# Optimization experiments

Measured on AMD Instinct MI355X. Metric: run time of the kernel, lower is better.

The kernel has to match this reference:

```python
import jax, jax.numpy as jnp
import numpy as np

N_NODES = 50000
N_EDGES = 1_600_000
IN_DIM = 512
HIDDEN = 512
OUT_DIM = 128
K = 10
ALPHA = 0.1


def setup_inputs() -> dict:
    key = jax.random.key(0)
    ks = jax.random.split(key, 7)
    x = jax.random.normal(ks[0], (N_NODES, IN_DIM), dtype=jnp.float32)
    edge_index = jax.random.randint(ks[1], (2, N_EDGES), 0, N_NODES, dtype=jnp.int64)
    s_in = 1.0 / np.sqrt(IN_DIM)
    s_h = 1.0 / np.sqrt(HIDDEN)
    lin_in_w = jax.random.uniform(ks[2], (HIDDEN, IN_DIM), jnp.float32, -s_in, s_in)
    lin_in_b = jax.random.uniform(ks[3], (HIDDEN,), jnp.float32, -s_in, s_in)
    lin_out_w = jax.random.uniform(ks[4], (OUT_DIM, HIDDEN), jnp.float32, -s_h, s_h)
    lin_out_b = jax.random.uniform(ks[5], (OUT_DIM,), jnp.float32, -s_h, s_h)
    # GPR init: alpha*(1-alpha)^k, normalized
    w = np.array([ALPHA * (1 - ALPHA) ** k for k in range(K + 1)], dtype=np.float32)
    gpr_weights = jnp.asarray(w / w.sum())
    return {
        "x": x, "edge_index": edge_index,
        "lin_in_w": lin_in_w, "lin_in_b": lin_in_b,
        "lin_out_w": lin_out_w, "lin_out_b": lin_out_b,
        "gpr_weights": gpr_weights,
    }


def reference(x, edge_index, lin_in_w, lin_in_b, lin_out_w, lin_out_b, gpr_weights):
    n = x.shape[0]
    loops = jnp.arange(n, dtype=edge_index.dtype)
    row = jnp.concatenate([edge_index[0], loops])  # [E+n]
    col = jnp.concatenate([edge_index[1], loops])
    # degree over rows (edge_index_sl[0]), clamped to >=1
    deg = jax.ops.segment_sum(jnp.ones_like(row, dtype=x.dtype), row, num_segments=n)
    dis = jnp.clip(deg, 1.0) ** -0.5  # deg^-0.5, [n]

    h = jax.nn.relu(x @ lin_in_w.T + lin_in_b)  # [n, hidden] (dropout = identity in eval)
    w = jax.nn.softmax(gpr_weights)  # [K+1]

    def step(carry, wk):
        h_prop, acc = carry
        hs = h_prop * dis[:, None]
        h_prop = jax.ops.segment_sum(hs[col], row, num_segments=n) * dis[:, None]
        return (h_prop, acc + wk * h_prop), None

    (_, h_final), _ = jax.lax.scan(step, (h, w[0] * h), w[1:])
    return h_final @ lin_out_w.T + lin_out_b
```

## Files before the change

kernel.cpp:

```cpp
#include <hip/hip_runtime.h>


#define SLOTS 96
#define NB2   98
#define BCAP  18432
#define CHUNK 4096

typedef __attribute__((ext_vector_type(8))) short short8;
typedef __attribute__((ext_vector_type(4))) float f32x4;

__device__ inline ushort f2bf(float f) {
    uint x = __float_as_uint(f);
    return (ushort)((x + 0x7fffu + ((x >> 16) & 1u)) >> 16);
}
__device__ inline float bflo(uint u) { return __uint_as_float(u << 16); }
__device__ inline float bfhi(uint u) { return __uint_as_float(u & 0xffff0000u); }

__device__ __forceinline__ void glds16(const ushort* g, ushort* l) {
    __builtin_amdgcn_global_load_lds(
        (const __attribute__((address_space(1))) void*)g,
        (__attribute__((address_space(3))) void*)l, 16, 0, 0);
}

__global__ void init_kernel(int* __restrict__ gcur, int ngc,
                            ushort* __restrict__ yAll, size_t ystride, int zrow,
                            const float* __restrict__ gpr, float* __restrict__ w11) {
    const int gid = blockIdx.x * blockDim.x + threadIdx.x;
    const int stride = gridDim.x * blockDim.x;
    if (gid == 0) {
        float m = gpr[0];
        for (int i = 1; i < 11; ++i) m = fmaxf(m, gpr[i]);
        float e[11], s = 0.f;
        for (int i = 0; i < 11; ++i) { e[i] = expf(gpr[i] - m); s += e[i]; }
        float inv = 1.f / s;
        for (int i = 0; i < 11; ++i) w11[i] = e[i] * inv;
    }
    for (int i = gid; i < ngc; i += stride) gcur[i] = 0;
    for (int i = gid; i < 11 * 128; i += stride) {
        int k = i >> 7, d = i & 127;
        yAll[(size_t)k * ystride + (size_t)zrow * 128 + d] = 0;
    }
}

__global__ __launch_bounds__(512) void partition_kernel(
    const int* __restrict__ row, const int* __restrict__ col,
    int* __restrict__ gcur, uint* __restrict__ bbuf, int E) {
    __shared__ int cnt[128];
    __shared__ int base[128];
    __shared__ int gbase[128];
    __shared__ uint sbuf[CHUNK];
    const int tid = threadIdx.x;
    const int e0 = blockIdx.x * CHUNK;
    if (tid < 128) cnt[tid] = 0;
    __syncthreads();
    int myb[8]; int myp[8]; uint mye[8];
#pragma unroll
    for (int j = 0; j < 8; ++j) {
        int i = e0 + tid + j * 512;
        myb[j] = -1;
        if (i < E) {
            int r = row[i];
            int c = col[i];
            myb[j] = r >> 9;
            mye[j] = ((uint)(r & 511) << 16) | (uint)c;
            myp[j] = atomicAdd(&cnt[myb[j]], 1);
        }
    }
    __syncthreads();
    if (tid < 128) base[tid] = cnt[tid];
    __syncthreads();
    for (int off = 1; off < 128; off <<= 1) {
        int v = 0;
        if (tid < 128 && tid >= off) v = base[tid - off];
        __syncthreads();
        if (tid < 128) base[tid] += v;
        __syncthreads();
    }
    if (tid < 128) base[tid] -= cnt[tid];
    __syncthreads();
    if (tid < NB2 && cnt[tid] > 0) gbase[tid] = atomicAdd(&gcur[tid], cnt[tid]);
    __syncthreads();
#pragma unroll
    for (int j = 0; j < 8; ++j)
        if (myb[j] >= 0) sbuf[base[myb[j]] + myp[j]] = mye[j];
    __syncthreads();
    const int wv = tid >> 6, lane = tid & 63;
    for (int b = wv; b < NB2; b += 8) {
        const int len = cnt[b], src = base[b], dst = gbase[b];
        for (int i = lane; i < len; i += 64) {
            int d = dst + i;
            if (d < BCAP) bbuf[(size_t)b * BCAP + d] = sbuf[src + i];
        }
    }
}

__global__ __launch_bounds__(1024) void expand2_kernel(
    const int* __restrict__ gcur, const uint* __restrict__ bbuf,
    ushort* __restrict__ col_s, int* __restrict__ deg,
    float* __restrict__ dis, float* __restrict__ dis2, float* __restrict__ rdis,
    int n) {
    __shared__ int cur[128];
    const int b = blockIdx.x >> 2;
    const int q = blockIdx.x & 3;
    const int tid = threadIdx.x;
    if (tid < 128) cur[tid] = 0;
    __syncthreads();
    int cb = gcur[b];
    if (cb > BCAP) cb = BCAP;
    const size_t bb = (size_t)b * BCAP;
    const int rlo = q * 128, rhi = rlo + 128;
    for (int i = tid; i < cb; i += 1024) {
        uint e = bbuf[bb + i];
        int rl = (int)(e >> 16);
        if (rl >= rlo && rl < rhi) {
            int p = atomicAdd(&cur[rl - rlo], 1);
            if (p < SLOTS)
                col_s[((size_t)(b * 512 + rl)) * SLOTS + p] = (ushort)(e & 0xffffu);
        }
    }
    __syncthreads();
    if (tid < 128) {
        int r = b * 512 + rlo + tid;
        if (r < n) {
            int d = cur[tid];
            deg[r] = d;
            float fd = (float)(d + 1);
            float di = rsqrtf(fd);
            dis[r] = di;
            dis2[r] = di * di;
            rdis[r] = sqrtf(fd);
            int pstart = d < SLOTS ? d : SLOTS;
            int pend = (pstart + 7) & ~7;
            if (pend > SLOTS) pend = SLOTS;
            ushort* cp = col_s + (size_t)r * SLOTS;
            for (int p = pstart; p < pend; ++p) cp[p] = (ushort)n;
        }
    }
}

__global__ void cvt_all_kernel(const float* __restrict__ x,
                               const float* __restrict__ win,
                               const float* __restrict__ wout,
                               ushort* __restrict__ x_bf,
                               ushort* __restrict__ win_bf,
                               ushort* __restrict__ wout_bf,
                               int nx_src8, int nx8, int nw18, int nw28) {
    const int gid = blockIdx.x * blockDim.x + threadIdx.x;
    const int stride = gridDim.x * blockDim.x;
    const int tot = nx8 + nw18 + nw28;
    for (int i = gid; i < tot; i += stride) {
        const float* src;
        ushort* dst;
        int idx;
        if (i < nx8) {
            if (i >= nx_src8) {
                short8 z = (short8)0;
                *reinterpret_cast<short8*>(x_bf + (size_t)i * 8) = z;
                continue;
            }
            src = x; dst = x_bf; idx = i;
        } else if (i < nx8 + nw18) {
            src = win; dst = win_bf; idx = i - nx8;
        } else {
            src = wout; dst = wout_bf; idx = i - nx8 - nw18;
        }
        const float4* s = reinterpret_cast<const float4*>(src + (size_t)idx * 8);
        float4 a = s[0], b = s[1];
        short8 o;
        o[0] = (short)f2bf(a.x); o[1] = (short)f2bf(a.y);
        o[2] = (short)f2bf(a.z); o[3] = (short)f2bf(a.w);
        o[4] = (short)f2bf(b.x); o[5] = (short)f2bf(b.y);
        o[6] = (short)f2bf(b.z); o[7] = (short)f2bf(b.w);
        *reinterpret_cast<short8*>(dst + (size_t)idx * 8) = o;
    }
}

__global__ __launch_bounds__(512) void gemm1_kernel(
    const ushort* __restrict__ A, const ushort* __restrict__ B,
    const float* __restrict__ bias, ushort* __restrict__ outH, int M) {
    __shared__ __align__(16) ushort As[128 * 32];
    __shared__ __align__(16) ushort Bs[256 * 32];
    const int tid = threadIdx.x;
    const int lane = tid & 63;
    const int w = tid >> 6;
    const int wm = (w >> 2) * 64, wn = (w & 3) * 64;
    const int bm = blockIdx.y * 128, bn = blockIdx.x * 256;
    const int lrow = lane & 15, lk8 = (lane >> 4) * 8;

    f32x4 acc[4][4];
#pragma unroll
    for (int i = 0; i < 4; ++i)
#pragma unroll
        for (int j = 0; j < 4; ++j) acc[i][j] = (f32x4)(0.f);

    const int arow = 16 * w + (lane >> 2);
    const int acol = (lane & 3) * 8;
    const ushort* gA = A + (size_t)(bm + arow) * 512 + acol;
    const ushort* gB0 = B + (size_t)(bn + 32 * w + (lane >> 2)) * 512 + acol;
    const ushort* gB1 = gB0 + (size_t)16 * 512;
    ushort* lA = As + w * 512;
    ushort* lB0 = Bs + w * 1024;
    ushort* lB1 = Bs + w * 1024 + 512;

    for (int k0 = 0; k0 < 512; k0 += 32) {
        glds16(gA + k0, lA);
        glds16(gB0 + k0, lB0);
        glds16(gB1 + k0, lB1);
        __syncthreads();
        short8 af[4], bfr[4];
#pragma unroll
        for (int mf = 0; mf < 4; ++mf)
            af[mf] = *reinterpret_cast<const short8*>(As + (wm + mf * 16 + lrow) * 32 + lk8);
#pragma unroll
        for (int nf = 0; nf < 4; ++nf)
            bfr[nf] = *reinterpret_cast<const short8*>(Bs + (wn + nf * 16 + lrow) * 32 + lk8);
#pragma unroll
        for (int mf = 0; mf < 4; ++mf)
#pragma unroll
            for (int nf = 0; nf < 4; ++nf)
                acc[mf][nf] = __builtin_amdgcn_mfma_f32_16x16x32_bf16(af[mf], bfr[nf], acc[mf][nf], 0, 0, 0);
        __syncthreads();
    }

#pragma unroll
    for (int mf = 0; mf < 4; ++mf) {
#pragma unroll
        for (int nf = 0; nf < 4; ++nf) {
            const int col = bn + wn + nf * 16 + lrow;
#pragma unroll
            for (int r = 0; r < 4; ++r) {
                const int row = bm + wm + mf * 16 + (lane >> 4) * 4 + r;
                if (row < M) {
                    float v = fmaxf(acc[mf][nf][r] + bias[col], 0.f);
                    outH[(size_t)row * 512 + col] = f2bf(v);
                }
            }
        }
    }
}

__global__ __launch_bounds__(256) void gemm2_kernel(
    const ushort* __restrict__ A, const ushort* __restrict__ B,
    const float* __restrict__ dis, ushort* __restrict__ outY, int M) {
    __shared__ __align__(16) ushort As[128 * 32];
    __shared__ __align__(16) ushort Bs[128 * 32];
    const int tid = threadIdx.x;
    const int lane = tid & 63;
    const int w = tid >> 6;
    const int wm = (w >> 1) * 64, wn = (w & 1) * 64;
    const int bm = blockIdx.x * 128;
    const int lrow = lane & 15, lk8 = (lane >> 4) * 8;

    f32x4 acc[4][4];
#pragma unroll
    for (int i = 0; i < 4; ++i)
#pragma unroll
        for (int j = 0; j < 4; ++j) acc[i][j] = (f32x4)(0.f);

    const int sub = 32 * w + (lane >> 2);
    const int acol = (lane & 3) * 8;
    const ushort* gA0 = A + (size_t)(bm + sub) * 512 + acol;
    const ushort* gA1 = gA0 + (size_t)16 * 512;
    const ushort* gB0 = B + (size_t)sub * 512 + acol;
    const ushort* gB1 = gB0 + (size_t)16 * 512;
    ushort* lA0 = As + w * 1024;
    ushort* lA1 = As + w * 1024 + 512;
    ushort* lB0 = Bs + w * 1024;
    ushort* lB1 = Bs + w * 1024 + 512;

    for (int k0 = 0; k0 < 512; k0 += 32) {
        glds16(gA0 + k0, lA0);
        glds16(gA1 + k0, lA1);
        glds16(gB0 + k0, lB0);
        glds16(gB1 + k0, lB1);
        __syncthreads();
        short8 af[4], bfr[4];
#pragma unroll
        for (int mf = 0; mf < 4; ++mf)
            af[mf] = *reinterpret_cast<const short8*>(As + (wm + mf * 16 + lrow) * 32 + lk8);
#pragma unroll
        for (int nf = 0; nf < 4; ++nf)
            bfr[nf] = *reinterpret_cast<const short8*>(Bs + (wn + nf * 16 + lrow) * 32 + lk8);
#pragma unroll
        for (int mf = 0; mf < 4; ++mf)
#pragma unroll
            for (int nf = 0; nf < 4; ++nf)
                acc[mf][nf] = __builtin_amdgcn_mfma_f32_16x16x32_bf16(af[mf], bfr[nf], acc[mf][nf], 0, 0, 0);
        __syncthreads();
    }

#pragma unroll
    for (int mf = 0; mf < 4; ++mf) {
#pragma unroll
        for (int nf = 0; nf < 4; ++nf) {
            const int col = wn + nf * 16 + lrow;
#pragma unroll
            for (int r = 0; r < 4; ++r) {
                const int row = bm + wm + mf * 16 + (lane >> 4) * 4 + r;
                if (row < M)
                    outY[(size_t)row * 128 + col] = f2bf(dis[row] * acc[mf][nf][r]);
            }
        }
    }
}

__global__ __launch_bounds__(256) void spmm128_kernel(
    const int* __restrict__ deg, const ushort* __restrict__ col_s,
    const float* __restrict__ dis2,
    const ushort* __restrict__ y_old, ushort* __restrict__ y_new, int n) {
    int wid = (blockIdx.x * 256 + threadIdx.x) >> 6;
    if (wid >= n) return;
    wid = __builtin_amdgcn_readfirstlane(wid);
    const int lane = threadIdx.x & 63;
    int cnt = deg[wid];
    if (cnt > SLOTS) cnt = SLOTS;
    const int cnt8 = (cnt + 7) & ~7;
    const ushort* __restrict__ cp = col_s + (size_t)wid * SLOTS;
    const uint* __restrict__ Y = reinterpret_cast<const uint*>(y_old);
    float s0a = 0.f, s1a = 0.f, s0b = 0.f, s1b = 0.f;
    int t = 0;
    for (; t + 16 <= cnt8; t += 16) {
        int c[16];
        uint v[16];
#pragma unroll
        for (int j = 0; j < 16; ++j) c[j] = (int)cp[t + j];
#pragma unroll
        for (int j = 0; j < 16; ++j) v[j] = Y[(size_t)c[j] * 64 + lane];
#pragma unroll
        for (int j = 0; j < 16; ++j) {
            if (j & 1) { s0b += bflo(v[j]); s1b += bfhi(v[j]); }
            else       { s0a += bflo(v[j]); s1a += bfhi(v[j]); }
        }
    }
    if (t < cnt8) {
        int c[8];
        uint v[8];
#pragma unroll
        for (int j = 0; j < 8; ++j) c[j] = (int)cp[t + j];
#pragma unroll
        for (int j = 0; j < 8; ++j) v[j] = Y[(size_t)c[j] * 64 + lane];
#pragma unroll
        for (int j = 0; j < 8; ++j) {
            if (j & 1) { s0b += bflo(v[j]); s1b += bfhi(v[j]); }
            else       { s0a += bflo(v[j]); s1a += bfhi(v[j]); }
        }
    }
    const uint u = Y[(size_t)wid * 64 + lane];
    const float d2 = dis2[wid];
    const float y0 = d2 * (bflo(u) + (s0a + s0b));
    const float y1 = d2 * (bfhi(u) + (s1a + s1b));
    reinterpret_cast<uint*>(y_new)[(size_t)wid * 64 + lane] =
        (uint)f2bf(y0) | ((uint)f2bf(y1) << 16);
}

__global__ __launch_bounds__(256) void spmm_last_kernel(
    const int* __restrict__ deg, const ushort* __restrict__ col_s,
    const float* __restrict__ dis2, const float* __restrict__ rdis,
    const ushort* __restrict__ yAll, size_t ystride_dw,
    const float* __restrict__ w11, const float* __restrict__ bout,
    float* __restrict__ outp, int n) {
    int wid = (blockIdx.x * 256 + threadIdx.x) >> 6;
    if (wid >= n) return;
    wid = __builtin_amdgcn_readfirstlane(wid);
    const int lane = threadIdx.x & 63;
    const uint* __restrict__ Y9 = reinterpret_cast<const uint*>(yAll) + 9 * ystride_dw;
    int cnt = deg[wid];
    if (cnt > SLOTS) cnt = SLOTS;
    const int cnt8 = (cnt + 7) & ~7;
    const ushort* __restrict__ cp = col_s + (size_t)wid * SLOTS;
    float s0a = 0.f, s1a = 0.f, s0b = 0.f, s1b = 0.f;
    int t = 0;
    for (; t + 16 <= cnt8; t += 16) {
        int c[16];
        uint v[16];
#pragma unroll
        for (int j = 0; j < 16; ++j) c[j] = (int)cp[t + j];
#pragma unroll
        for (int j = 0; j < 16; ++j) v[j] = Y9[(size_t)c[j] * 64 + lane];
#pragma unroll
        for (int j = 0; j < 16; ++j) {
            if (j & 1) { s0b += bflo(v[j]); s1b += bfhi(v[j]); }
            else       { s0a += bflo(v[j]); s1a += bfhi(v[j]); }
        }
    }
    if (t < cnt8) {
        int c[8];
        uint v[8];
#pragma unroll
        for (int j = 0; j < 8; ++j) c[j] = (int)cp[t + j];
#pragma unroll
        for (int j = 0; j < 8; ++j) v[j] = Y9[(size_t)c[j] * 64 + lane];
#pragma unroll
        for (int j = 0; j < 8; ++j) {
            if (j & 1) { s0b += bflo(v[j]); s1b += bfhi(v[j]); }
            else       { s0a += bflo(v[j]); s1a += bfhi(v[j]); }
        }
    }
    const uint u9 = Y9[(size_t)wid * 64 + lane];
    const float d2 = dis2[wid];
    const float y10_0 = d2 * (bflo(u9) + (s0a + s0b));
    const float y10_1 = d2 * (bfhi(u9) + (s1a + s1b));
    const float w10 = w11[10];
    float s0 = w10 * y10_0, s1 = w10 * y10_1;
    const uint* __restrict__ Y = reinterpret_cast<const uint*>(yAll);
#pragma unroll
    for (int k = 0; k < 10; ++k) {
        const uint v = Y[k * ystride_dw + (size_t)wid * 64 + lane];
        const float wk = w11[k];
        s0 = fmaf(wk, bflo(v), s0);
        s1 = fmaf(wk, bfhi(v), s1);
    }
    const float r = rdis[wid];
    float2 o;
    o.x = fmaf(s0, r, bout[lane * 2 + 0]);
    o.y = fmaf(s1, r, bout[lane * 2 + 1]);
    *reinterpret_cast<float2*>(outp + (size_t)wid * 128 + lane * 2) = o;
}

extern "C" void kernel_launch(void* const* d_in, const int* in_sizes, int n_in,
                              void* d_out, int out_size, void* d_ws, size_t ws_size,
                              hipStream_t stream) {
    const float* x    = (const float*)d_in[0];
    const int*   ei   = (const int*)d_in[1];
    const float* win  = (const float*)d_in[2];
    const float* bin  = (const float*)d_in[3];
    const float* wout = (const float*)d_in[4];
    const float* bout = (const float*)d_in[5];
    const float* gpr  = (const float*)d_in[6];
    float* out = (float*)d_out;

    const int n = in_sizes[0] / 512;
    const int E = in_sizes[1] / 2;
    const int Mpad = ((n + 127) / 128) * 128;
    const int NPAD = NB2 * 512;

    char* ws = (char*)d_ws;
    size_t off = 0;
    auto take = [&](size_t bytes) -> char* {
        char* p = ws + off;
        off += (bytes + 511) & ~(size_t)511;
        return p;
    };
    int*    deg     = (int*)take((size_t)n * sizeof(int));
    float*  dis     = (float*)take((size_t)n * sizeof(float));
    float*  dis2    = (float*)take((size_t)n * sizeof(float));
    float*  rdis    = (float*)take((size_t)n * sizeof(float));
    float*  w11     = (float*)take(16 * sizeof(float));
    int*    gcur    = (int*)take(128 * sizeof(int));
    uint*   bbuf    = (uint*)take((size_t)NB2 * BCAP * sizeof(uint));
    ushort* col_s   = (ushort*)take((size_t)NPAD * SLOTS * sizeof(ushort));
    ushort* x_bf    = (ushort*)take((size_t)Mpad * 512 * sizeof(ushort));
    ushort* win_bf  = (ushort*)take((size_t)512 * 512 * sizeof(ushort));
    ushort* wout_bf = (ushort*)take((size_t)128 * 512 * sizeof(ushort));
    ushort* h_bf    = (ushort*)take((size_t)Mpad * 512 * sizeof(ushort));
    const size_t ystride = (size_t)Mpad * 128;
    ushort* yAll    = (ushort*)take(11 * ystride * sizeof(ushort));

    const int* rowp = ei;
    const int* colp = ei + E;

    init_kernel<<<64, 256, 0, stream>>>(gcur, 128, yAll, ystride, n, gpr, w11);
    partition_kernel<<<(E + CHUNK - 1) / CHUNK, 512, 0, stream>>>(rowp, colp, gcur, bbuf, E);
    expand2_kernel<<<NB2 * 4, 1024, 0, stream>>>(gcur, bbuf, col_s, deg, dis, dis2, rdis, n);

    cvt_all_kernel<<<2048, 256, 0, stream>>>(x, win, wout, x_bf, win_bf, wout_bf,
                                             n * 64, Mpad * 64, 512 * 64, 128 * 64);

    dim3 g1(2, Mpad / 128);
    gemm1_kernel<<<g1, 512, 0, stream>>>(x_bf, win_bf, bin, h_bf, n);

    gemm2_kernel<<<Mpad / 128, 256, 0, stream>>>(h_bf, wout_bf, dis, yAll, n);

    const int spmm_blocks = (n + 3) / 4;
    for (int k = 1; k <= 9; ++k) {
        spmm128_kernel<<<spmm_blocks, 256, 0, stream>>>(
            deg, col_s, dis2, yAll + (size_t)(k - 1) * ystride, yAll + (size_t)k * ystride, n);
    }

    spmm_last_kernel<<<spmm_blocks, 256, 0, stream>>>(
        deg, col_s, dis2, rdis, yAll, ystride / 2, w11, bout, out, n);
}
```

Before: 631.6 us.

## Split propagation features into four 32-column slices for cache-resident SpMM

Stores the propagated feature matrix as four separate 32-column slices, each 64 bytes per row, and runs the full 10-step propagation chain per slice. Each wave splits into four 16-lane groups that gather different neighbours, then combines the partial sums with cross-lane shuffles. The aim is to keep each slice's working set (about 3.2 MB) resident in L2/LLC so random neighbour gathers hit cache instead of HBM. The cost is four times as many kernel launches, four re-reads of the column index lists, and only 16 of 64 lanes doing the final stores.

```diff
diff --git a/kernel.cpp b/kernel.cpp
--- a/kernel.cpp
+++ b/kernel.cpp
@@ -23,7 +23,7 @@
 }
 
 __global__ void init_kernel(int* __restrict__ gcur, int ngc,
-                            ushort* __restrict__ yAll, size_t ystride, int zrow,
+                            uint* __restrict__ yAll, size_t ss32, int zrow,
                             const float* __restrict__ gpr, float* __restrict__ w11) {
     const int gid = blockIdx.x * blockDim.x + threadIdx.x;
     const int stride = gridDim.x * blockDim.x;
@@ -36,9 +36,9 @@
         for (int i = 0; i < 11; ++i) w11[i] = e[i] * inv;
     }
     for (int i = gid; i < ngc; i += stride) gcur[i] = 0;
-    for (int i = gid; i < 11 * 128; i += stride) {
-        int k = i >> 7, d = i & 127;
-        yAll[(size_t)k * ystride + (size_t)zrow * 128 + d] = 0;
+    for (int i = gid; i < 44 * 16; i += stride) {
+        int sk = i >> 4, f = i & 15;
+        yAll[(size_t)sk * ss32 + (size_t)zrow * 16 + f] = 0;
     }
 }
 
@@ -241,7 +241,8 @@
 
 __global__ __launch_bounds__(256) void gemm2_kernel(
     const ushort* __restrict__ A, const ushort* __restrict__ B,
-    const float* __restrict__ dis, ushort* __restrict__ outY, int M) {
+    const float* __restrict__ dis, ushort* __restrict__ outY,
+    size_t chain16, int M) {
     __shared__ __align__(16) ushort As[128 * 32];
     __shared__ __align__(16) ushort Bs[128 * 32];
     const int tid = threadIdx.x;
@@ -294,127 +295,126 @@
 #pragma unroll
         for (int nf = 0; nf < 4; ++nf) {
             const int col = wn + nf * 16 + lrow;
+            const size_t sbase = (size_t)(col >> 5) * chain16 + (col & 31);
 #pragma unroll
             for (int r = 0; r < 4; ++r) {
                 const int row = bm + wm + mf * 16 + (lane >> 4) * 4 + r;
                 if (row < M)
-                    outY[(size_t)row * 128 + col] = f2bf(dis[row] * acc[mf][nf][r]);
+                    outY[sbase + (size_t)row * 32] = f2bf(dis[row] * acc[mf][nf][r]);
             }
         }
     }
 }
 
-__global__ __launch_bounds__(256) void spmm128_kernel(
+__global__ __launch_bounds__(256) void spmm_slice_kernel(
     const int* __restrict__ deg, const ushort* __restrict__ col_s,
     const float* __restrict__ dis2,
-    const ushort* __restrict__ y_old, ushort* __restrict__ y_new, int n) {
+    const uint* __restrict__ y_old, uint* __restrict__ y_new, int n) {
     int wid = (blockIdx.x * 256 + threadIdx.x) >> 6;
     if (wid >= n) return;
     wid = __builtin_amdgcn_readfirstlane(wid);
     const int lane = threadIdx.x & 63;
+    const int grp = lane >> 4, fl = lane & 15;
     int cnt = deg[wid];
     if (cnt > SLOTS) cnt = SLOTS;
     const int cnt8 = (cnt + 7) & ~7;
     const ushort* __restrict__ cp = col_s + (size_t)wid * SLOTS;
-    const uint* __restrict__ Y = reinterpret_cast<const uint*>(y_old);
-    float s0a = 0.f, s1a = 0.f, s0b = 0.f, s1b = 0.f;
+    float s0 = 0.f, s1 = 0.f;
     int t = 0;
     for (; t + 16 <= cnt8; t += 16) {
-        int c[16];
-        uint v[16];
-#pragma unroll
-        for (int j = 0; j < 16; ++j) c[j] = (int)cp[t + j];
-#pragma unroll
-        for (int j = 0; j < 16; ++j) v[j] = Y[(size_t)c[j] * 64 + lane];
-#pragma unroll
-        for (int j = 0; j < 16; ++j) {
-            if (j & 1) { s0b += bflo(v[j]); s1b += bfhi(v[j]); }
-            else       { s0a += bflo(v[j]); s1a += bfhi(v[j]); }
-        }
+        const int myc = (int)cp[t + (lane & 15)];
+        int c[4];
+        uint v[4];
+#pragma unroll
+        for (int i = 0; i < 4; ++i) c[i] = __shfl(myc, i * 4 + grp);
+#pragma unroll
+        for (int i = 0; i < 4; ++i) v[i] = y_old[(size_t)c[i] * 16 + fl];
+#pragma unroll
+        for (int i = 0; i < 4; ++i) { s0 += bflo(v[i]); s1 += bfhi(v[i]); }
     }
     if (t < cnt8) {
-        int c[8];
-        uint v[8];
-#pragma unroll
-        for (int j = 0; j < 8; ++j) c[j] = (int)cp[t + j];
-#pragma unroll
-        for (int j = 0; j < 8; ++j) v[j] = Y[(size_t)c[j] * 64 + lane];
-#pragma unroll
-        for (int j = 0; j < 8; ++j) {
-            if (j & 1) { s0b += bflo(v[j]); s1b += bfhi(v[j]); }
-            else       { s0a += bflo(v[j]); s1a += bfhi(v[j]); }
-        }
-    }
-    const uint u = Y[(size_t)wid * 64 + lane];
+        const int myc = (int)cp[t + (lane & 7)];
+        int c[2];
+        uint v[2];
+#pragma unroll
+        for (int i = 0; i < 2; ++i) c[i] = __shfl(myc, i * 4 + grp);
+#pragma unroll
+        for (int i = 0; i < 2; ++i) v[i] = y_old[(size_t)c[i] * 16 + fl];
+#pragma unroll
+        for (int i = 0; i < 2; ++i) { s0 += bflo(v[i]); s1 += bfhi(v[i]); }
+    }
+    s0 += __shfl_xor(s0, 16); s1 += __shfl_xor(s1, 16);
+    s0 += __shfl_xor(s0, 32); s1 += __shfl_xor(s1, 32);
+    const uint u = y_old[(size_t)wid * 16 + fl];
     const float d2 = dis2[wid];
-    const float y0 = d2 * (bflo(u) + (s0a + s0b));
-    const float y1 = d2 * (bfhi(u) + (s1a + s1b));
-    reinterpret_cast<uint*>(y_new)[(size_t)wid * 64 + lane] =
-        (uint)f2bf(y0) | ((uint)f2bf(y1) << 16);
-}
-
-__global__ __launch_bounds__(256) void spmm_last_kernel(
+    const float y0 = d2 * (bflo(u) + s0);
+    const float y1 = d2 * (bfhi(u) + s1);
+    if (lane < 16)
+        y_new[(size_t)wid * 16 + fl] = (uint)f2bf(y0) | ((uint)f2bf(y1) << 16);
+}
+
+__global__ __launch_bounds__(256) void spmm_last_slice_kernel(
     const int* __restrict__ deg, const ushort* __restrict__ col_s,
     const float* __restrict__ dis2, const float* __restrict__ rdis,
-    const ushort* __restrict__ yAll, size_t ystride_dw,
+    const uint* __restrict__ yChain, size_t ss32,
     const float* __restrict__ w11, const float* __restrict__ bout,
-    float* __restrict__ outp, int n) {
+    float* __restrict__ outp, int colbase, int n) {
     int wid = (blockIdx.x * 256 + threadIdx.x) >> 6;
     if (wid >= n) return;
     wid = __builtin_amdgcn_readfirstlane(wid);
     const int lane = threadIdx.x & 63;
-    const uint* __restrict__ Y9 = reinterpret_cast<const uint*>(yAll) + 9 * ystride_dw;
+    const int grp = lane >> 4, fl = lane & 15;
+    const uint* __restrict__ Y9 = yChain + 9 * ss32;
     int cnt = deg[wid];
     if (cnt > SLOTS) cnt = SLOTS;
     const int cnt8 = (cnt + 7) & ~7;
     const ushort* __restrict__ cp = col_s + (size_t)wid * SLOTS;
-    float s0a = 0.f, s1a = 0.f, s0b = 0.f, s1b = 0.f;
+    float s0 = 0.f, s1 = 0.f;
     int t = 0;
     for (; t + 16 <= cnt8; t += 16) {
-        int c[16];
-        uint v[16];
-#pragma unroll
-        for (int j = 0; j < 16; ++j) c[j] = (int)cp[t + j];
-#pragma unroll
-        for (int j = 0; j < 16; ++j) v[j] = Y9[(size_t)c[j] * 64 + lane];
-#pragma unroll
-        for (int j = 0; j < 16; ++j) {
-            if (j & 1) { s0b += bflo(v[j]); s1b += bfhi(v[j]); }
-            else       { s0a += bflo(v[j]); s1a += bfhi(v[j]); }
-        }
+        const int myc = (int)cp[t + (lane & 15)];
+        int c[4];
+        uint v[4];
+#pragma unroll
+        for (int i = 0; i < 4; ++i) c[i] = __shfl(myc, i * 4 + grp);
+#pragma unroll
+        for (int i = 0; i < 4; ++i) v[i] = Y9[(size_t)c[i] * 16 + fl];
+#pragma unroll
+        for (int i = 0; i < 4; ++i) { s0 += bflo(v[i]); s1 += bfhi(v[i]); }
     }
     if (t < cnt8) {
-        int c[8];
-        uint v[8];
-#pragma unroll
-        for (int j = 0; j < 8; ++j) c[j] = (int)cp[t + j];
-#pragma unroll
-        for (int j = 0; j < 8; ++j) v[j] = Y9[(size_t)c[j] * 64 + lane];
-#pragma unroll
-        for (int j = 0; j < 8; ++j) {
-            if (j & 1) { s0b += bflo(v[j]); s1b += bfhi(v[j]); }
-            else       { s0a += bflo(v[j]); s1a += bfhi(v[j]); }
-        }
-    }
-    const uint u9 = Y9[(size_t)wid * 64 + lane];
+        const int myc = (int)cp[t + (lane & 7)];
+        int c[2];
+        uint v[2];
+#pragma unroll
+        for (int i = 0; i < 2; ++i) c[i] = __shfl(myc, i * 4 + grp);
+#pragma unroll
+        for (int i = 0; i < 2; ++i) v[i] = Y9[(size_t)c[i] * 16 + fl];
+#pragma unroll
+        for (int i = 0; i < 2; ++i) { s0 += bflo(v[i]); s1 += bfhi(v[i]); }
+    }
+    s0 += __shfl_xor(s0, 16); s1 += __shfl_xor(s1, 16);
+    s0 += __shfl_xor(s0, 32); s1 += __shfl_xor(s1, 32);
+    const uint u9 = Y9[(size_t)wid * 16 + fl];
     const float d2 = dis2[wid];
-    const float y10_0 = d2 * (bflo(u9) + (s0a + s0b));
-    const float y10_1 = d2 * (bfhi(u9) + (s1a + s1b));
+    const float y10_0 = d2 * (bflo(u9) + s0);
+    const float y10_1 = d2 * (bfhi(u9) + s1);
     const float w10 = w11[10];
-    float s0 = w10 * y10_0, s1 = w10 * y10_1;
-    const uint* __restrict__ Y = reinterpret_cast<const uint*>(yAll);
+    float a0 = w10 * y10_0, a1 = w10 * y10_1;
 #pragma unroll
     for (int k = 0; k < 10; ++k) {
-        const uint v = Y[k * ystride_dw + (size_t)wid * 64 + lane];
+        const uint v = yChain[k * ss32 + (size_t)wid * 16 + fl];
         const float wk = w11[k];
-        s0 = fmaf(wk, bflo(v), s0);
-        s1 = fmaf(wk, bfhi(v), s1);
+        a0 = fmaf(wk, bflo(v), a0);
+        a1 = fmaf(wk, bfhi(v), a1);
     }
     const float r = rdis[wid];
+    const int cc = colbase + fl * 2;
     float2 o;
-    o.x = fmaf(s0, r, bout[lane * 2 + 0]);
-    o.y = fmaf(s1, r, bout[lane * 2 + 1]);
-    *reinterpret_cast<float2*>(outp + (size_t)wid * 128 + lane * 2) = o;
+    o.x = fmaf(a0, r, bout[cc + 0]);
+    o.y = fmaf(a1, r, bout[cc + 1]);
+    if (lane < 16)
+        *reinterpret_cast<float2*>(outp + (size_t)wid * 128 + cc) = o;
 }
 
 extern "C" void kernel_launch(void* const* d_in, const int* in_sizes, int n_in,
@@ -433,6 +433,9 @@
     const int E = in_sizes[1] / 2;
     const int Mpad = ((n + 127) / 128) * 128;
     const int NPAD = NB2 * 512;
+    const size_t ss32 = (size_t)Mpad * 16;
+    const size_t chain32 = 11 * ss32;
+    const size_t chain16 = 2 * chain32;
 
     char* ws = (char*)d_ws;
     size_t off = 0;
@@ -453,13 +456,12 @@
     ushort* win_bf  = (ushort*)take((size_t)512 * 512 * sizeof(ushort));
     ushort* wout_bf = (ushort*)take((size_t)128 * 512 * sizeof(ushort));
     ushort* h_bf    = (ushort*)take((size_t)Mpad * 512 * sizeof(ushort));
-    const size_t ystride = (size_t)Mpad * 128;
-    ushort* yAll    = (ushort*)take(11 * ystride * sizeof(ushort));
+    uint*   yAll    = (uint*)take(4 * chain32 * sizeof(uint));
 
     const int* rowp = ei;
     const int* colp = ei + E;
 
-    init_kernel<<<64, 256, 0, stream>>>(gcur, 128, yAll, ystride, n, gpr, w11);
+    init_kernel<<<64, 256, 0, stream>>>(gcur, 128, yAll, ss32, n, gpr, w11);
     partition_kernel<<<(E + CHUNK - 1) / CHUNK, 512, 0, stream>>>(rowp, colp, gcur, bbuf, E);
     expand2_kernel<<<NB2 * 4, 1024, 0, stream>>>(gcur, bbuf, col_s, deg, dis, dis2, rdis, n);
 
@@ -469,14 +471,18 @@
     dim3 g1(2, Mpad / 128);
     gemm1_kernel<<<g1, 512, 0, stream>>>(x_bf, win_bf, bin, h_bf, n);
 
-    gemm2_kernel<<<Mpad / 128, 256, 0, stream>>>(h_bf, wout_bf, dis, yAll, n);
+    gemm2_kernel<<<Mpad / 128, 256, 0, stream>>>(h_bf, wout_bf, dis,
+                                                 (ushort*)yAll, chain16, n);
 
     const int spmm_blocks = (n + 3) / 4;
-    for (int k = 1; k <= 9; ++k) {
-        spmm128_kernel<<<spmm_blocks, 256, 0, stream>>>(
-            deg, col_s, dis2, yAll + (size_t)(k - 1) * ystride, yAll + (size_t)k * ystride, n);
-    }
-
-    spmm_last_kernel<<<spmm_blocks, 256, 0, stream>>>(
-        deg, col_s, dis2, rdis, yAll, ystride / 2, w11, bout, out, n);
-}
+    for (int s = 0; s < 4; ++s) {
+        const uint* chain = yAll + (size_t)s * chain32;
+        for (int k = 1; k <= 9; ++k) {
+            spmm_slice_kernel<<<spmm_blocks, 256, 0, stream>>>(
+                deg, col_s, dis2, chain + (size_t)(k - 1) * ss32,
+                (uint*)(chain + (size_t)k * ss32), n);
+        }
+        spmm_last_slice_kernel<<<spmm_blocks, 256, 0, stream>>>(
+            deg, col_s, dis2, rdis, chain, ss32, w11, bout, out, s * 32, n);
+    }
+}
```

New measurement: 991.7 us. 57.0% more time.
